# Optimization experiments

Measured on AMD Instinct MI355X. Metric: run time of the kernel, lower is better.

Reference implementation:

```python
import jax, jax.numpy as jnp
import numpy as np

NUM_OPS, B, T, D = 8, 8, 512, 1024


def setup_inputs() -> dict:
    key = jax.random.key(0)
    k1, k2, k3, k4 = jax.random.split(key, 4)
    x = jax.random.normal(k1, (B, T, D), dtype=jnp.float32)
    W = jax.random.normal(k2, (NUM_OPS, D, D), dtype=jnp.float32) * 0.02
    b = jnp.zeros((NUM_OPS, D), dtype=jnp.float32)
    logits = 0.001 * jax.random.normal(k3, (NUM_OPS,), dtype=jnp.float32)
    # uniform noise for Gumbel sampling (matches tf.random.uniform in sample_without_replacement)
    u = jax.random.uniform(k4, (NUM_OPS,), dtype=jnp.float32, minval=1e-6, maxval=1.0 - 1e-6)
    return {"x": x, "W": W, "b": b, "logits": logits, "u": u}


def reference(x, W, b, logits, u):
    # weights = softmax(logits); gumbel top-1 over log(weights) == log_softmax(logits)
    gumbel = -jnp.log(-jnp.log(u))
    idx = jnp.argmax(jax.nn.log_softmax(logits) + gumbel)
    # forward of ops_times_mask_binary: sum over ON ops (num_on_samples=1 -> single op)
    out = jnp.einsum('btd,de->bte', x, W[idx]) + b[idx]  # [B,T,D]
    return out
```

## Files before the change

### kernel.cpp

```cpp
#include <hip/hip_runtime.h>

typedef unsigned short u16;
typedef __attribute__((ext_vector_type(8))) short bf16x8;
typedef __attribute__((ext_vector_type(4))) float f32x4;

#define NUM_OPS 8
#define M_DIM 4096
#define K_DIM 1024
#define N_DIM 1024


__device__ __forceinline__ u16 f2b(float f) {
  union { float f; unsigned u; } v; v.f = f;
  unsigned r = v.u + 0x7fffu + ((v.u >> 16) & 1u);
  return (u16)(r >> 16);
}

__device__ __forceinline__ int compute_idx(const float* __restrict__ logits,
                                           const float* __restrict__ u) {
  int best = 0; float bv = -3.4e38f;
#pragma unroll
  for (int i = 0; i < NUM_OPS; ++i) {
    float g = -logf(-logf(u[i]));
    float v = logits[i] + g;
    if (v > bv) { bv = v; best = i; }
  }
  return best;
}

__device__ __forceinline__ void gld_lds16(const void* g, void* l) {
  __builtin_amdgcn_global_load_lds(
      (__attribute__((address_space(1))) void*)(g),
      (__attribute__((address_space(3))) void*)(unsigned)(unsigned long long)(l),
      16, 0, 0);
}

__global__ void prep_kernel(const float* __restrict__ x, const float* __restrict__ W,
                            const float* __restrict__ logits, const float* __restrict__ u,
                            u16* __restrict__ xb, u16* __restrict__ wt) {
  const int tid = threadIdx.x;
  const int bid = blockIdx.x;
  if (bid < 2048) {
    size_t i0 = ((size_t)bid * 256 + tid) * 8;
    const float4* xp = (const float4*)(x + i0);
    float4 f0 = xp[0], f1 = xp[1];
    unsigned p0 = (unsigned)f2b(f0.x) | ((unsigned)f2b(f0.y) << 16);
    unsigned p1 = (unsigned)f2b(f0.z) | ((unsigned)f2b(f0.w) << 16);
    unsigned p2 = (unsigned)f2b(f1.x) | ((unsigned)f2b(f1.y) << 16);
    unsigned p3 = (unsigned)f2b(f1.z) | ((unsigned)f2b(f1.w) << 16);
    uint4 pk; pk.x = p0; pk.y = p1; pk.z = p2; pk.w = p3;
    *(uint4*)(xb + i0) = pk;
  } else {
    __shared__ u16 t[64][66];
    const int wb = bid - 2048;
    const int kt = wb >> 4, nt = wb & 15;
    const int idx = compute_idx(logits, u);
    const float* Wi = W + (size_t)idx * K_DIM * N_DIM;
#pragma unroll
    for (int it = 0; it < 16; ++it) {
      int i = it * 256 + tid;
      int r = i >> 6, c = i & 63;
      t[r][c] = f2b(Wi[(size_t)(kt * 64 + r) * N_DIM + nt * 64 + c]);
    }
    __syncthreads();
#pragma unroll
    for (int it = 0; it < 16; ++it) {
      int i = it * 256 + tid;
      int n = i >> 6, k = i & 63;
      wt[(size_t)(nt * 64 + n) * K_DIM + kt * 64 + k] = t[k][n];
    }
  }
}

__global__ __launch_bounds__(256) void gemm_kernel(
    const u16* __restrict__ xb, const u16* __restrict__ wt,
    const float* __restrict__ bvec, const float* __restrict__ logits,
    const float* __restrict__ u, float* __restrict__ out) {
  __shared__ u16 sA[2][128 * 32];
  __shared__ u16 sB[2][128 * 32];

  const int tid = threadIdx.x;
  const int w = tid >> 6, L = tid & 63;
  const int m0 = blockIdx.y * 128;
  const int n0 = blockIdx.x * 128;

  const int q0 = 2 * w, q1 = 2 * w + 1;
  const int rlo = (L >> 2), cofs = (L & 3) * 8;
  const u16* gA0 = xb + (size_t)(m0 + 16 * q0 + rlo) * K_DIM + cofs;
  const u16* gA1 = xb + (size_t)(m0 + 16 * q1 + rlo) * K_DIM + cofs;
  const u16* gB0 = wt + (size_t)(n0 + 16 * q0 + rlo) * K_DIM + cofs;
  const u16* gB1 = wt + (size_t)(n0 + 16 * q1 + rlo) * K_DIM + cofs;
  const int lofs0 = q0 * 512 + L * 8;
  const int lofs1 = q1 * 512 + L * 8;

  const int wm = w & 1, wn = w >> 1;
  int aoff[4], boff[4];
#pragma unroll
  for (int t = 0; t < 4; ++t) {
    aoff[t] = (64 * wm + 16 * t + (L & 15)) * 32 + (L >> 4) * 8;
    boff[t] = (64 * wn + 16 * t + (L & 15)) * 32 + (L >> 4) * 8;
  }

  f32x4 acc[4][4] = {};

  gld_lds16(gA0, &sA[0][lofs0]);
  gld_lds16(gA1, &sA[0][lofs1]);
  gld_lds16(gB0, &sB[0][lofs0]);
  gld_lds16(gB1, &sB[0][lofs1]);
  __syncthreads();

  for (int kk = 0; kk < K_DIM / 32; ++kk) {
    const int cur = kk & 1, nxt = cur ^ 1;
    if (kk + 1 < K_DIM / 32) {
      const int ko = (kk + 1) * 32;
      gld_lds16(gA0 + ko, &sA[nxt][lofs0]);
      gld_lds16(gA1 + ko, &sA[nxt][lofs1]);
      gld_lds16(gB0 + ko, &sB[nxt][lofs0]);
      gld_lds16(gB1 + ko, &sB[nxt][lofs1]);
    }

    bf16x8 af[4], bf[4];
#pragma unroll
    for (int t = 0; t < 4; ++t) {
      af[t] = *(const bf16x8*)(&sA[cur][0] + aoff[t]);
      bf[t] = *(const bf16x8*)(&sB[cur][0] + boff[t]);
    }
#pragma unroll
    for (int mt = 0; mt < 4; ++mt)
#pragma unroll
      for (int nt = 0; nt < 4; ++nt)
        acc[mt][nt] = __builtin_amdgcn_mfma_f32_16x16x32_bf16(
            af[mt], bf[nt], acc[mt][nt], 0, 0, 0);

    __syncthreads();
  }

  const int idx = compute_idx(logits, u);
  const float* bi = bvec + (size_t)idx * N_DIM;
#pragma unroll
  for (int mt = 0; mt < 4; ++mt) {
    int row = m0 + 64 * wm + 16 * mt + (L >> 4) * 4;
#pragma unroll
    for (int nt = 0; nt < 4; ++nt) {
      int col = n0 + 64 * wn + 16 * nt + (L & 15);
      float bv = bi[col];
#pragma unroll
      for (int r = 0; r < 4; ++r)
        out[(size_t)(row + r) * N_DIM + col] = acc[mt][nt][r] + bv;
    }
  }
}


extern "C" void kernel_launch(void* const* d_in, const int* in_sizes, int n_in,
                              void* d_out, int out_size, void* d_ws, size_t ws_size,
                              hipStream_t stream) {
  const float* x      = (const float*)d_in[0];
  const float* W      = (const float*)d_in[1];
  const float* bvec   = (const float*)d_in[2];
  const float* logits = (const float*)d_in[3];
  const float* u      = (const float*)d_in[4];
  float* out = (float*)d_out;

  u16* xb = (u16*)d_ws;
  u16* wt = (u16*)d_ws + (size_t)M_DIM * K_DIM;

  prep_kernel<<<2048 + 256, 256, 0, stream>>>(x, W, logits, u, xb, wt);
  dim3 grid(N_DIM / 128, M_DIM / 128);
  gemm_kernel<<<grid, 256, 0, stream>>>(xb, wt, bvec, logits, u, out);
}
```

Baseline: 118.5 us.

## Pre-tile bf16 operands into MFMA fragment order and remap GEMM block ordering

The prep kernel now writes x and the transposed W in a tiled 16x32 chunk layout that matches the MFMA fragment order. Each GEMM global-to-LDS load then reads one contiguous 1KB chunk, and LDS fragment reads become linear, which is meant to remove LDS bank conflicts and strided global loads. The GEMM also switches to a 1D grid with a swizzled block-to-tile mapping for better L2 reuse, and moves the barrier to the top of the loop. The weight transpose reads LDS column-wise to pack eight values per thread, which may add LDS conflicts in prep.

```diff
diff --git a/kernel.cpp b/kernel.cpp
--- a/kernel.cpp
+++ b/kernel.cpp
@@ -1,6 +1,7 @@
 #include <hip/hip_runtime.h>
 
 typedef unsigned short u16;
+typedef unsigned int u32;
 typedef __attribute__((ext_vector_type(8))) short bf16x8;
 typedef __attribute__((ext_vector_type(4))) float f32x4;
 
@@ -8,12 +9,18 @@
 #define M_DIM 4096
 #define K_DIM 1024
 #define N_DIM 1024
+#define BK 32
+#define KITERS (K_DIM / BK)
 
 
 __device__ __forceinline__ u16 f2b(float f) {
-  union { float f; unsigned u; } v; v.f = f;
-  unsigned r = v.u + 0x7fffu + ((v.u >> 16) & 1u);
+  union { float f; u32 u; } v; v.f = f;
+  u32 r = v.u + 0x7fffu + ((v.u >> 16) & 1u);
   return (u16)(r >> 16);
+}
+
+__device__ __forceinline__ u32 pk2(float a, float b) {
+  return (u32)f2b(a) | ((u32)f2b(b) << 16);
 }
 
 __device__ __forceinline__ int compute_idx(const float* __restrict__ logits,
@@ -21,8 +28,7 @@
   int best = 0; float bv = -3.4e38f;
 #pragma unroll
   for (int i = 0; i < NUM_OPS; ++i) {
-    float g = -logf(-logf(u[i]));
-    float v = logits[i] + g;
+    float v = logits[i] - logf(-logf(u[i]));
     if (v > bv) { bv = v; best = i; }
   }
   return best;
@@ -41,15 +47,16 @@
   const int tid = threadIdx.x;
   const int bid = blockIdx.x;
   if (bid < 2048) {
-    size_t i0 = ((size_t)bid * 256 + tid) * 8;
-    const float4* xp = (const float4*)(x + i0);
-    float4 f0 = xp[0], f1 = xp[1];
-    unsigned p0 = (unsigned)f2b(f0.x) | ((unsigned)f2b(f0.y) << 16);
-    unsigned p1 = (unsigned)f2b(f0.z) | ((unsigned)f2b(f0.w) << 16);
-    unsigned p2 = (unsigned)f2b(f1.x) | ((unsigned)f2b(f1.y) << 16);
-    unsigned p3 = (unsigned)f2b(f1.z) | ((unsigned)f2b(f1.w) << 16);
-    uint4 pk; pk.x = p0; pk.y = p1; pk.z = p2; pk.w = p3;
-    *(uint4*)(xb + i0) = pk;
+    const int chunk = bid * 4 + (tid >> 6), l = tid & 63;
+    const int mtile = chunk >> 5, ktile = chunk & 31;
+    const float* src = x + (size_t)(mtile * 16 + (l & 15)) * K_DIM
+                         + ktile * 32 + (l >> 4) * 8;
+    float4 f0 = *(const float4*)(src);
+    float4 f1 = *(const float4*)(src + 4);
+    uint4 p;
+    p.x = pk2(f0.x, f0.y); p.y = pk2(f0.z, f0.w);
+    p.z = pk2(f1.x, f1.y); p.w = pk2(f1.z, f1.w);
+    *(uint4*)(xb + (size_t)chunk * 512 + l * 8) = p;
   } else {
     __shared__ u16 t[64][66];
     const int wb = bid - 2048;
@@ -64,10 +71,18 @@
     }
     __syncthreads();
 #pragma unroll
-    for (int it = 0; it < 16; ++it) {
-      int i = it * 256 + tid;
-      int n = i >> 6, k = i & 63;
-      wt[(size_t)(nt * 64 + n) * K_DIM + kt * 64 + k] = t[k][n];
+    for (int it = 0; it < 2; ++it) {
+      int s = it * 256 + tid;
+      int c = s >> 6, l = s & 63;
+      int ntl = c & 3, ktl = c >> 2;
+      int kb = ktl * 32 + (l >> 4) * 8, nn = ntl * 16 + (l & 15);
+      uint4 p;
+      p.x = (u32)t[kb + 0][nn] | ((u32)t[kb + 1][nn] << 16);
+      p.y = (u32)t[kb + 2][nn] | ((u32)t[kb + 3][nn] << 16);
+      p.z = (u32)t[kb + 4][nn] | ((u32)t[kb + 5][nn] << 16);
+      p.w = (u32)t[kb + 6][nn] | ((u32)t[kb + 7][nn] << 16);
+      int chunk = (nt * 4 + ntl) * 32 + (kt * 2 + ktl);
+      *(uint4*)(wt + (size_t)chunk * 512 + l * 8) = p;
     }
   }
 }
@@ -76,54 +91,55 @@
     const u16* __restrict__ xb, const u16* __restrict__ wt,
     const float* __restrict__ bvec, const float* __restrict__ logits,
     const float* __restrict__ u, float* __restrict__ out) {
-  __shared__ u16 sA[2][128 * 32];
-  __shared__ u16 sB[2][128 * 32];
+  __shared__ u16 sA[2][8 * 512];
+  __shared__ u16 sB[2][8 * 512];
 
   const int tid = threadIdx.x;
   const int w = tid >> 6, L = tid & 63;
-  const int m0 = blockIdx.y * 128;
-  const int n0 = blockIdx.x * 128;
+  const int bid = blockIdx.x;
+  const int mb = (bid & 7) * 4 + (bid >> 6);
+  const int nb = (bid >> 3) & 7;
+  const int m0 = mb * 128, n0 = nb * 128;
 
-  const int q0 = 2 * w, q1 = 2 * w + 1;
-  const int rlo = (L >> 2), cofs = (L & 3) * 8;
-  const u16* gA0 = xb + (size_t)(m0 + 16 * q0 + rlo) * K_DIM + cofs;
-  const u16* gA1 = xb + (size_t)(m0 + 16 * q1 + rlo) * K_DIM + cofs;
-  const u16* gB0 = wt + (size_t)(n0 + 16 * q0 + rlo) * K_DIM + cofs;
-  const u16* gB1 = wt + (size_t)(n0 + 16 * q1 + rlo) * K_DIM + cofs;
-  const int lofs0 = q0 * 512 + L * 8;
-  const int lofs1 = q1 * 512 + L * 8;
+  const int c0 = 2 * w, c1 = 2 * w + 1;
+  const u16* gA0 = xb + ((size_t)((mb * 8 + c0) * 32)) * 512 + L * 8;
+  const u16* gA1 = xb + ((size_t)((mb * 8 + c1) * 32)) * 512 + L * 8;
+  const u16* gB0 = wt + ((size_t)((nb * 8 + c0) * 32)) * 512 + L * 8;
+  const u16* gB1 = wt + ((size_t)((nb * 8 + c1) * 32)) * 512 + L * 8;
+  const int lA0 = c0 * 512 + L * 8, lA1 = c1 * 512 + L * 8;
 
   const int wm = w & 1, wn = w >> 1;
   int aoff[4], boff[4];
 #pragma unroll
   for (int t = 0; t < 4; ++t) {
-    aoff[t] = (64 * wm + 16 * t + (L & 15)) * 32 + (L >> 4) * 8;
-    boff[t] = (64 * wn + 16 * t + (L & 15)) * 32 + (L >> 4) * 8;
+    aoff[t] = (4 * wm + t) * 512 + L * 8;
+    boff[t] = (4 * wn + t) * 512 + L * 8;
   }
 
   f32x4 acc[4][4] = {};
 
-  gld_lds16(gA0, &sA[0][lofs0]);
-  gld_lds16(gA1, &sA[0][lofs1]);
-  gld_lds16(gB0, &sB[0][lofs0]);
-  gld_lds16(gB1, &sB[0][lofs1]);
-  __syncthreads();
+  gld_lds16(gA0, &sA[0][lA0]);
+  gld_lds16(gA1, &sA[0][lA1]);
+  gld_lds16(gB0, &sB[0][lA0]);
+  gld_lds16(gB1, &sB[0][lA1]);
 
-  for (int kk = 0; kk < K_DIM / 32; ++kk) {
+  for (int kk = 0; kk < KITERS; ++kk) {
     const int cur = kk & 1, nxt = cur ^ 1;
-    if (kk + 1 < K_DIM / 32) {
-      const int ko = (kk + 1) * 32;
-      gld_lds16(gA0 + ko, &sA[nxt][lofs0]);
-      gld_lds16(gA1 + ko, &sA[nxt][lofs1]);
-      gld_lds16(gB0 + ko, &sB[nxt][lofs0]);
-      gld_lds16(gB1 + ko, &sB[nxt][lofs1]);
+    __syncthreads();
+
+    if (kk + 1 < KITERS) {
+      const int ko = (kk + 1) * 512;
+      gld_lds16(gA0 + ko, &sA[nxt][lA0]);
+      gld_lds16(gA1 + ko, &sA[nxt][lA1]);
+      gld_lds16(gB0 + ko, &sB[nxt][lA0]);
+      gld_lds16(gB1 + ko, &sB[nxt][lA1]);
     }
 
     bf16x8 af[4], bf[4];
 #pragma unroll
     for (int t = 0; t < 4; ++t) {
-      af[t] = *(const bf16x8*)(&sA[cur][0] + aoff[t]);
-      bf[t] = *(const bf16x8*)(&sB[cur][0] + boff[t]);
+      af[t] = *(const bf16x8*)(&sA[cur][aoff[t]]);
+      bf[t] = *(const bf16x8*)(&sB[cur][boff[t]]);
     }
 #pragma unroll
     for (int mt = 0; mt < 4; ++mt)
@@ -131,8 +147,6 @@
       for (int nt = 0; nt < 4; ++nt)
         acc[mt][nt] = __builtin_amdgcn_mfma_f32_16x16x32_bf16(
             af[mt], bf[nt], acc[mt][nt], 0, 0, 0);
-
-    __syncthreads();
   }
 
   const int idx = compute_idx(logits, u);
@@ -166,6 +180,5 @@
   u16* wt = (u16*)d_ws + (size_t)M_DIM * K_DIM;
 
   prep_kernel<<<2048 + 256, 256, 0, stream>>>(x, W, logits, u, xb, wt);
-  dim3 grid(N_DIM / 128, M_DIM / 128);
-  gemm_kernel<<<grid, 256, 0, stream>>>(xb, wt, bvec, logits, u, out);
+  gemm_kernel<<<256, 256, 0, stream>>>(xb, wt, bvec, logits, u, out);
 }
```

Result: faster. 112.2 us (-5.3%).
